# Optimization experiments

Measured on AMD Instinct MI355X. Metric: run time of the kernel, lower is better.

Reference implementation:

```python
import jax, jax.numpy as jnp
import numpy as np

DIM = 512
NUM_HEADS = 8
HEAD_DIM = DIM // NUM_HEADS
SCALE = HEAD_DIM ** -0.5


def setup_inputs() -> dict:
    key = jax.random.key(0)
    kx, kqw, kqb, kpw, kpb = jax.random.split(key, 5)
    B, N = 2, 4096
    x = jax.random.normal(kx, (B, N, DIM), dtype=jnp.float32)
    # nn.Linear weights stored as [out, in]; init ~ U(-1/sqrt(in), 1/sqrt(in))
    bound = 1.0 / np.sqrt(DIM)
    qkv_w = jax.random.uniform(kqw, (3 * DIM, DIM), minval=-bound, maxval=bound, dtype=jnp.float32)
    qkv_b = jax.random.uniform(kqb, (3 * DIM,), minval=-bound, maxval=bound, dtype=jnp.float32)
    proj_w = jax.random.uniform(kpw, (DIM, DIM), minval=-bound, maxval=bound, dtype=jnp.float32)
    proj_b = jax.random.uniform(kpb, (DIM,), minval=-bound, maxval=bound, dtype=jnp.float32)
    return {"x": x, "qkv_w": qkv_w, "qkv_b": qkv_b, "proj_w": proj_w, "proj_b": proj_b}


def reference(x, qkv_w, qkv_b, proj_w, proj_b):
    B, N, C = x.shape
    # qkv: [B, N, 3C] -> [3, B, H, N, Dh]
    qkv = x @ qkv_w.T + qkv_b
    qkv = qkv.reshape(B, N, 3, NUM_HEADS, HEAD_DIM).transpose(2, 0, 3, 1, 4)
    q, k, v = qkv[0], qkv[1], qkv[2]
    # scores: [B, H, N, N] (materialized, matching the original math)
    attn = jnp.einsum("bhqd,bhkd->bhqk", q, k) * SCALE
    attn = jax.nn.softmax(attn, axis=-1)
    out = jnp.einsum("bhqk,bhkd->bhqd", attn, v)  # [B, H, N, Dh]
    out = out.transpose(0, 2, 1, 3).reshape(B, N, C)
    return out @ proj_w.T + proj_b
```

## Files before the change

kernel.cpp:

```cpp
#include <hip/hip_runtime.h>
#include <hip/hip_bf16.h>
#include <stdint.h>
#include <stddef.h>

typedef __attribute__((ext_vector_type(8))) short short8;
typedef __attribute__((ext_vector_type(4))) float f32x4;
typedef __attribute__((ext_vector_type(16))) float f32x16;

#define MFMA16(a, b, c) __builtin_amdgcn_mfma_f32_16x16x32_bf16((a), (b), (c), 0, 0, 0)
#define MFMA32(a, b, c) __builtin_amdgcn_mfma_f32_32x32x16_bf16((a), (b), (c), 0, 0, 0)

#define QSCALE 0.1803368801111204f

#if __has_builtin(__builtin_amdgcn_exp2f)
#define EXP2(x) __builtin_amdgcn_exp2f(x)
#else
#define EXP2(x) __builtin_exp2f(x)
#endif

__device__ __forceinline__ float b2f(short x) {
    unsigned u = ((unsigned)(unsigned short)x) << 16;
    float f; __builtin_memcpy(&f, &u, 4); return f;
}
__device__ __forceinline__ short f2b(float f) {
    unsigned u; __builtin_memcpy(&u, &f, 4);
    u = (u + 0x7FFFu + ((u >> 16) & 1u)) >> 16;
    return (short)u;
}
__device__ __forceinline__ unsigned pack2(float a, float b) {
    unsigned ua, ub; __builtin_memcpy(&ua, &a, 4); __builtin_memcpy(&ub, &b, 4);
    return __builtin_amdgcn_perm(ub + 0x8000u, ua + 0x8000u, 0x07060302u);
}
__device__ __forceinline__ unsigned cvtpk(float a, float b) {
    unsigned r;
    asm("v_cvt_pk_bf16_f32 %0, %1, %2" : "=v"(r) : "v"(a), "v"(b));
    return r;
}
__device__ __forceinline__ short8 load8f(const float* p) {
    const float4 f0 = *(const float4*)p;
    const float4 f1 = *(const float4*)(p + 4);
    short8 r;
    r[0]=f2b(f0.x); r[1]=f2b(f0.y); r[2]=f2b(f0.z); r[3]=f2b(f0.w);
    r[4]=f2b(f1.x); r[5]=f2b(f1.y); r[6]=f2b(f1.z); r[7]=f2b(f1.w);
    return r;
}

__global__ __launch_bounds__(256) void cvt3(
    const float* __restrict__ s0, short* __restrict__ d0, int n0,
    const float* __restrict__ s1, short* __restrict__ d1, int n1,
    const float* __restrict__ s2, short* __restrict__ d2, int n2)
{
    int i = blockIdx.x * 256 + threadIdx.x;
    if (i < n0) { *(short8*)(d0 + (size_t)i * 8) = load8f(s0 + (size_t)i * 8); return; }
    i -= n0;
    if (i < n1) { *(short8*)(d1 + (size_t)i * 8) = load8f(s1 + (size_t)i * 8); return; }
    i -= n1;
    if (i < n2) { *(short8*)(d2 + (size_t)i * 8) = load8f(s2 + (size_t)i * 8); }
}

__global__ __launch_bounds__(256) void qkv_gemm(
    const short* __restrict__ X, const short* __restrict__ W,
    const float* __restrict__ bias,
    short* __restrict__ Qb, short* __restrict__ Kb, short* __restrict__ Vb)
{
    __shared__ short sT[128][132];

    const int tid  = threadIdx.x;
    const int wv   = tid >> 6;
    const int lane = tid & 63;
    const int l15  = lane & 15;
    const int quad = lane >> 4;
    const int m0   = blockIdx.x * 128 + (wv >> 1) * 64;
    const int sec  = blockIdx.y >> 2;
    const int bis  = blockIdx.y & 3;
    const int nbase = sec * 512 + bis * 128;
    const int j0   = (wv & 1) * 64;

    const f32x4 zero = {0.f, 0.f, 0.f, 0.f};
    f32x4 acc[4][4];
#pragma unroll
    for (int i = 0; i < 4; i++)
#pragma unroll
        for (int j = 0; j < 4; j++) acc[i][j] = zero;

    for (int k0 = 0; k0 < 512; k0 += 32) {
        short8 a[4], b[4];
#pragma unroll
        for (int i = 0; i < 4; i++)
            a[i] = *(const short8*)(X + (size_t)(m0 + i * 16 + l15) * 512 + k0 + quad * 8);
#pragma unroll
        for (int j = 0; j < 4; j++)
            b[j] = *(const short8*)(W + (size_t)(nbase + j0 + j * 16 + l15) * 512 + k0 + quad * 8);
#pragma unroll
        for (int i = 0; i < 4; i++)
#pragma unroll
            for (int j = 0; j < 4; j++)
                acc[i][j] = MFMA16(a[i], b[j], acc[i][j]);
    }

    if (sec < 2) {
        const float scale = (sec == 0) ? QSCALE : 1.0f;
        short* dst = (sec == 0) ? Qb : Kb;
#pragma unroll
        for (int j = 0; j < 4; j++) {
            const int jcl = j0 + j * 16 + l15;
            const float bs = bias[sec * 512 + bis * 128 + jcl];
#pragma unroll
            for (int i = 0; i < 4; i++) {
                const int s0 = (wv >> 1) * 64 + i * 16 + quad * 4;
#pragma unroll
                for (int r = 0; r < 4; r++)
                    sT[s0 + r][jcl] = f2b((acc[i][j][r] + bs) * scale);
            }
        }
        __syncthreads();

        const int seqlocal = tid & 127;
        const int hl_loc   = tid >> 7;
        const int hl  = bis * 2 + hl_loc;
        const int m   = blockIdx.x * 128 + seqlocal;
        const int bb  = m >> 12, seqg = m & 4095;
        short* drow = dst + ((size_t)(bb * 8 + hl) * 4096 + seqg) * 64;
#pragma unroll
        for (int u = 0; u < 8; u++)
            *(short8*)(drow + u * 8) = *(const short8*)&sT[seqlocal][hl_loc * 64 + u * 8];
    } else {
#pragma unroll
        for (int j = 0; j < 4; j++) {
            const int jcl = j0 + j * 16 + l15;
            const float bs = bias[nbase + jcl];
#pragma unroll
            for (int i = 0; i < 4; i++) {
                uint2 w;
                w.x = pack2(acc[i][j][0] + bs, acc[i][j][1] + bs);
                w.y = pack2(acc[i][j][2] + bs, acc[i][j][3] + bs);
                *(uint2*)&sT[jcl][(wv >> 1) * 64 + i * 16 + quad * 4] = w;
            }
        }
        __syncthreads();

        const int jcl = tid >> 1, half = tid & 1;
        const int hl = (bis * 128 + jcl) >> 6;
        const int d  = jcl & 63;
        const int bb = (blockIdx.x * 128) >> 12;
        const int seq0 = ((blockIdx.x * 128) & 4095) + half * 64;
        short* dst = Vb + ((size_t)(bb * 8 + hl) * 64 + d) * 4096 + seq0;
#pragma unroll
        for (int u = 0; u < 8; u++)
            *(short8*)(dst + u * 8) = *(const short8*)&sT[jcl][half * 64 + u * 8];
    }
}

__global__ __launch_bounds__(512, 4) void flash_attn(
    const short* __restrict__ Q, const short* __restrict__ K,
    const short* __restrict__ V, short* __restrict__ PO0,
    short* __restrict__ PO1, float* __restrict__ lbuf, int niter)
{
    __shared__ short sK[2][128][72];
    __shared__ short sV[2][64][136];

    const int tid  = threadIdx.x;
    const int wv   = tid >> 6;
    const int lane = tid & 63;
    const int l31  = lane & 31;
    const int half = lane >> 5;
    const int bh = blockIdx.y;
    const int b = bh >> 3, h = bh & 7;
    const int qw = blockIdx.x * 256 + wv * 32;
    const int ks = blockIdx.z;
    const int key0 = ks * niter * 128;

    const short* Qb = Q + (size_t)bh * 4096 * 64;
    const short* Kb = K + (size_t)bh * 4096 * 64;
    const short* Vb = V + (size_t)bh * 64 * 4096;

    short8 aq[4];
#pragma unroll
    for (int s = 0; s < 4; s++)
        aq[s] = *(const short8*)(Qb + (size_t)(qw + l31) * 64 + s * 16 + half * 8);

    f32x16 o0 = {}, o1 = {};
    float la0 = 0.f, la1 = 0.f, la2 = 0.f, la3 = 0.f;

    const int r0  = tid >> 3;
    const int scb = (tid & 7) * 8;
    const int vb  = (scb & ~12) | ((scb & 8) >> 1);

    short8 pk0, pk1, pv0, pv1;
    pk0 = *(const short8*)(Kb + (size_t)(key0 + r0) * 64 + scb);
    pk1 = *(const short8*)(Kb + (size_t)(key0 + 64 + r0) * 64 + scb);
    pv0 = *(const short8*)(Vb + (size_t)r0 * 4096 + key0 + scb);
    pv1 = *(const short8*)(Vb + (size_t)r0 * 4096 + key0 + 64 + scb);
    *(short8*)&sK[0][r0][scb]      = pk0;
    *(short8*)&sK[0][64 + r0][scb] = pk1;
    *(uint2*)&sV[0][r0][vb]          = ((const uint2*)&pv0)[0];
    *(uint2*)&sV[0][r0][vb + 8]      = ((const uint2*)&pv0)[1];
    *(uint2*)&sV[0][r0][64 + vb]     = ((const uint2*)&pv1)[0];
    *(uint2*)&sV[0][r0][64 + vb + 8] = ((const uint2*)&pv1)[1];
    {
        const int kn = key0 + 128;
        pk0 = *(const short8*)(Kb + (size_t)(kn + r0) * 64 + scb);
        pk1 = *(const short8*)(Kb + (size_t)(kn + 64 + r0) * 64 + scb);
        pv0 = *(const short8*)(Vb + (size_t)r0 * 4096 + kn + scb);
        pv1 = *(const short8*)(Vb + (size_t)r0 * 4096 + kn + 64 + scb);
    }

    for (int kt = 0; kt < niter; ++kt) {
        __syncthreads();

        if (kt + 1 < niter) {
            short (*sKn)[72]  = sK[(kt + 1) & 1];
            short (*sVn)[136] = sV[(kt + 1) & 1];
            *(short8*)&sKn[r0][scb]      = pk0;
            *(short8*)&sKn[64 + r0][scb] = pk1;
            *(uint2*)&sVn[r0][vb]          = ((const uint2*)&pv0)[0];
            *(uint2*)&sVn[r0][vb + 8]      = ((const uint2*)&pv0)[1];
            *(uint2*)&sVn[r0][64 + vb]     = ((const uint2*)&pv1)[0];
            *(uint2*)&sVn[r0][64 + vb + 8] = ((const uint2*)&pv1)[1];
        }
        if (kt + 2 < niter) {
            const int kn = key0 + (kt + 2) * 128;
            pk0 = *(const short8*)(Kb + (size_t)(kn + r0) * 64 + scb);
            pk1 = *(const short8*)(Kb + (size_t)(kn + 64 + r0) * 64 + scb);
            pv0 = *(const short8*)(Vb + (size_t)r0 * 4096 + kn + scb);
            pv1 = *(const short8*)(Vb + (size_t)r0 * 4096 + kn + 64 + scb);
        }

        const short (*sKc)[72]  = sK[kt & 1];
        const short (*sVc)[136] = sV[kt & 1];

#pragma unroll
        for (int i = 0; i < 4; i++) {
            const int c = (i + wv) & 3;
            f32x16 ST = {};
            __builtin_amdgcn_s_setprio(1);
#pragma unroll
            for (int s = 0; s < 4; s++) {
                const short8 bk = *(const short8*)&sKc[c * 32 + l31][s * 16 + half * 8];
                ST = MFMA32(bk, aq[s], ST);
            }
            __builtin_amdgcn_s_setprio(0);
            float e[16];
#pragma unroll
            for (int r = 0; r < 16; r++) e[r] = EXP2(ST[r]);
            la0 += (e[0] + e[1]) + (e[2] + e[3]);
            la1 += (e[4] + e[5]) + (e[6] + e[7]);
            la2 += (e[8] + e[9]) + (e[10] + e[11]);
            la3 += (e[12] + e[13]) + (e[14] + e[15]);
            uint4 w0 = { cvtpk(e[0], e[1]),   cvtpk(e[2], e[3]),
                         cvtpk(e[4], e[5]),   cvtpk(e[6], e[7]) };
            uint4 w1 = { cvtpk(e[8], e[9]),   cvtpk(e[10], e[11]),
                         cvtpk(e[12], e[13]), cvtpk(e[14], e[15]) };
            const short8 bp0 = *(const short8*)&w0;
            const short8 bp1 = *(const short8*)&w1;

            __builtin_amdgcn_s_setprio(1);
            const short8 bv00 = *(const short8*)&sVc[l31][(2 * c) * 16 + half * 8];
            const short8 bv01 = *(const short8*)&sVc[32 + l31][(2 * c) * 16 + half * 8];
            o0 = MFMA32(bv00, bp0, o0);
            o1 = MFMA32(bv01, bp0, o1);
            const short8 bv10 = *(const short8*)&sVc[l31][(2 * c + 1) * 16 + half * 8];
            const short8 bv11 = *(const short8*)&sVc[32 + l31][(2 * c + 1) * 16 + half * 8];
            o0 = MFMA32(bv10, bp1, o0);
            o1 = MFMA32(bv11, bp1, o1);
            __builtin_amdgcn_s_setprio(0);
        }
    }

    float lsum = (la0 + la1) + (la2 + la3);
    lsum += __shfl_xor(lsum, 32);
    const float inv = 1.f / fmaxf(lsum, 1e-30f);

    short* PO = (ks == 0) ? PO0 : PO1;
#pragma unroll
    for (int q = 0; q < 4; q++) {
        uint2 w0, w1;
        w0.x = pack2(o0[4 * q + 0] * inv, o0[4 * q + 1] * inv);
        w0.y = pack2(o0[4 * q + 2] * inv, o0[4 * q + 3] * inv);
        w1.x = pack2(o1[4 * q + 0] * inv, o1[4 * q + 1] * inv);
        w1.y = pack2(o1[4 * q + 2] * inv, o1[4 * q + 3] * inv);
        const size_t rowoff = ((size_t)b * 4096 + qw + l31) * 512;
        const int col = h * 64 + q * 8 + half * 4;
        *(uint2*)(PO + rowoff + col) = w0;
        *(uint2*)(PO + rowoff + col + 32) = w1;
    }
    if (half == 0)
        lbuf[((size_t)ks * 16 + bh) * 4096 + qw + l31] = lsum;
}

__global__ __launch_bounds__(256) void combine(
    const short* __restrict__ PO0, const short* __restrict__ PO1,
    short* __restrict__ attn, const float* __restrict__ L)
{
    const int i = blockIdx.x * 256 + threadIdx.x;
    const size_t flat = (size_t)i * 8;
    const int col = (int)(flat & 511);
    const int q   = (int)((flat >> 9) & 4095);
    const int b   = (int)(flat >> 21);
    const int bh  = b * 8 + (col >> 6);
    const float l0 = L[(size_t)bh * 4096 + q];
    const float l1 = L[(size_t)65536 + (size_t)bh * 4096 + q];
    const float inv = 1.f / (l0 + l1);
    const float w0 = l0 * inv, w1 = l1 * inv;
    const short8 a = *(const short8*)(PO0 + flat);
    const short8 c = *(const short8*)(PO1 + flat);
    short8 r;
#pragma unroll
    for (int k = 0; k < 8; k += 2) {
        const unsigned p = pack2(w0 * b2f(a[k]) + w1 * b2f(c[k]),
                                 w0 * b2f(a[k + 1]) + w1 * b2f(c[k + 1]));
        r[k]     = (short)(p & 0xFFFF);
        r[k + 1] = (short)(p >> 16);
    }
    *(short8*)(attn + flat) = r;
}

__global__ __launch_bounds__(256) void proj_gemm(
    const short* __restrict__ A, const short* __restrict__ W,
    const float* __restrict__ bias, float* __restrict__ dst)
{
    const int tid  = threadIdx.x;
    const int wv   = tid >> 6;
    const int lane = tid & 63;
    const int l15  = lane & 15;
    const int quad = lane >> 4;
    const int m0 = blockIdx.x * 128 + (wv >> 1) * 64;
    const int n0 = blockIdx.y * 128 + (wv & 1) * 64;

    const f32x4 zero = {0.f, 0.f, 0.f, 0.f};
    f32x4 acc[4][4];
#pragma unroll
    for (int i = 0; i < 4; i++)
#pragma unroll
        for (int j = 0; j < 4; j++) acc[i][j] = zero;

    for (int k0 = 0; k0 < 512; k0 += 32) {
        short8 a[4], b[4];
#pragma unroll
        for (int i = 0; i < 4; i++)
            a[i] = *(const short8*)(A + (size_t)(m0 + i * 16 + l15) * 512 + k0 + quad * 8);
#pragma unroll
        for (int j = 0; j < 4; j++)
            b[j] = *(const short8*)(W + (size_t)(n0 + j * 16 + l15) * 512 + k0 + quad * 8);
#pragma unroll
        for (int i = 0; i < 4; i++)
#pragma unroll
            for (int j = 0; j < 4; j++)
                acc[i][j] = MFMA16(a[i], b[j], acc[i][j]);
    }

#pragma unroll
    for (int j = 0; j < 4; j++) {
        const int n = n0 + j * 16 + l15;
        const float bs = bias[n];
#pragma unroll
        for (int i = 0; i < 4; i++) {
#pragma unroll
            for (int r = 0; r < 4; r++) {
                const int m = m0 + i * 16 + quad * 4 + r;
                dst[(size_t)m * 512 + n] = acc[i][j][r] + bs;
            }
        }
    }
}

extern "C" void kernel_launch(void* const* d_in, const int* in_sizes, int n_in,
                              void* d_out, int out_size, void* d_ws, size_t ws_size,
                              hipStream_t stream)
{
    const float* x      = (const float*)d_in[0];
    const float* qkv_w  = (const float*)d_in[1];
    const float* qkv_b  = (const float*)d_in[2];
    const float* proj_w = (const float*)d_in[3];
    const float* proj_b = (const float*)d_in[4];

    const size_t MB = 1024 * 1024;
    short* xb   = (short*)d_out;
    short* wb   = (short*)d_out + 4 * MB;
    short* PO0  = (short*)d_out;
    short* PO1  = (short*)d_out + 4 * MB;
    float* out  = (float*)d_out;

    short* Qf = (short*)d_ws;
    short* Kf = Qf + (size_t)16 * 4096 * 64;
    short* Vf = Kf + (size_t)16 * 4096 * 64;
    short* attn = Qf;
    float* lbuf = (float*)((char*)d_ws + 24 * MB);
    short* pwb  = (short*)((char*)d_ws + 24 * MB + 512 * 1024);

    cvt3<<<2560, 256, 0, stream>>>(x, xb, 524288, qkv_w, wb, 98304, proj_w, pwb, 32768);
    qkv_gemm<<<dim3(64, 12), 256, 0, stream>>>(xb, wb, qkv_b, Qf, Kf, Vf);
    flash_attn<<<dim3(16, 16, 2), 512, 0, stream>>>(Qf, Kf, Vf, PO0, PO1, lbuf, 16);
    combine<<<2048, 256, 0, stream>>>(PO0, PO1, attn, lbuf);
    proj_gemm<<<dim3(64, 4), 256, 0, stream>>>(attn, pwb, proj_b, out);
}
```

Baseline: 230.6 us.

## Prefetch GEMM operands, compute softmax row sums via MFMA, retile projection GEMM

Both GEMM kernels now load the next k-slice's operands into registers before issuing the current MFMAs, so global load latency overlaps with compute. The flash attention kernel drops its scalar row-sum accumulation and shuffle, and instead sums the probabilities with an extra MFMA against a vector of bf16 ones. The projection GEMM uses smaller 64x128 tiles, twice as many blocks, and swapped MFMA operands so each lane writes float4 outputs with vectorized bias loads. The costs are higher register pressure from double-buffered operands, extra MFMA work in the attention inner loop, and a row sum taken from bf16-rounded probabilities rather than fp32 values.

```diff
diff --git a/kernel.cpp b/kernel.cpp
--- a/kernel.cpp
+++ b/kernel.cpp
@@ -83,19 +83,32 @@
 #pragma unroll
         for (int j = 0; j < 4; j++) acc[i][j] = zero;
 
+    const short* Arow = X + (size_t)(m0 + l15) * 512 + quad * 8;
+    const short* Brow = W + (size_t)(nbase + j0 + l15) * 512 + quad * 8;
+
+    short8 a[4], b[4];
+#pragma unroll
+    for (int i = 0; i < 4; i++) a[i] = *(const short8*)(Arow + (size_t)i * 16 * 512);
+#pragma unroll
+    for (int j = 0; j < 4; j++) b[j] = *(const short8*)(Brow + (size_t)j * 16 * 512);
+
+#pragma unroll 2
     for (int k0 = 0; k0 < 512; k0 += 32) {
-        short8 a[4], b[4];
-#pragma unroll
-        for (int i = 0; i < 4; i++)
-            a[i] = *(const short8*)(X + (size_t)(m0 + i * 16 + l15) * 512 + k0 + quad * 8);
-#pragma unroll
-        for (int j = 0; j < 4; j++)
-            b[j] = *(const short8*)(W + (size_t)(nbase + j0 + j * 16 + l15) * 512 + k0 + quad * 8);
+        const int kn = (k0 + 32 < 512) ? k0 + 32 : 0;
+        short8 an[4], bn[4];
+#pragma unroll
+        for (int i = 0; i < 4; i++) an[i] = *(const short8*)(Arow + (size_t)i * 16 * 512 + kn);
+#pragma unroll
+        for (int j = 0; j < 4; j++) bn[j] = *(const short8*)(Brow + (size_t)j * 16 * 512 + kn);
 #pragma unroll
         for (int i = 0; i < 4; i++)
 #pragma unroll
             for (int j = 0; j < 4; j++)
                 acc[i][j] = MFMA16(a[i], b[j], acc[i][j]);
+#pragma unroll
+        for (int i = 0; i < 4; i++) a[i] = an[i];
+#pragma unroll
+        for (int j = 0; j < 4; j++) b[j] = bn[j];
     }
 
     if (sec < 2) {
@@ -179,8 +192,12 @@
     for (int s = 0; s < 4; s++)
         aq[s] = *(const short8*)(Qb + (size_t)(qw + l31) * 64 + s * 16 + half * 8);
 
+    short8 ones;
+#pragma unroll
+    for (int j = 0; j < 8; j++) ones[j] = (short)0x3F80;
+
     f32x16 o0 = {}, o1 = {};
-    float la0 = 0.f, la1 = 0.f, la2 = 0.f, la3 = 0.f;
+    f32x16 o2 = {};
 
     const int r0  = tid >> 3;
     const int scb = (tid & 7) * 8;
@@ -243,10 +260,6 @@
             float e[16];
 #pragma unroll
             for (int r = 0; r < 16; r++) e[r] = EXP2(ST[r]);
-            la0 += (e[0] + e[1]) + (e[2] + e[3]);
-            la1 += (e[4] + e[5]) + (e[6] + e[7]);
-            la2 += (e[8] + e[9]) + (e[10] + e[11]);
-            la3 += (e[12] + e[13]) + (e[14] + e[15]);
             uint4 w0 = { cvtpk(e[0], e[1]),   cvtpk(e[2], e[3]),
                          cvtpk(e[4], e[5]),   cvtpk(e[6], e[7]) };
             uint4 w1 = { cvtpk(e[8], e[9]),   cvtpk(e[10], e[11]),
@@ -259,16 +272,17 @@
             const short8 bv01 = *(const short8*)&sVc[32 + l31][(2 * c) * 16 + half * 8];
             o0 = MFMA32(bv00, bp0, o0);
             o1 = MFMA32(bv01, bp0, o1);
+            o2 = MFMA32(ones, bp0, o2);
             const short8 bv10 = *(const short8*)&sVc[l31][(2 * c + 1) * 16 + half * 8];
             const short8 bv11 = *(const short8*)&sVc[32 + l31][(2 * c + 1) * 16 + half * 8];
             o0 = MFMA32(bv10, bp1, o0);
             o1 = MFMA32(bv11, bp1, o1);
+            o2 = MFMA32(ones, bp1, o2);
             __builtin_amdgcn_s_setprio(0);
         }
     }
 
-    float lsum = (la0 + la1) + (la2 + la3);
-    lsum += __shfl_xor(lsum, 32);
+    const float lsum = o2[0];
     const float inv = 1.f / fmaxf(lsum, 1e-30f);
 
     short* PO = (ks == 0) ? PO0 : PO1;
@@ -324,42 +338,57 @@
     const int lane = tid & 63;
     const int l15  = lane & 15;
     const int quad = lane >> 4;
-    const int m0 = blockIdx.x * 128 + (wv >> 1) * 64;
-    const int n0 = blockIdx.y * 128 + (wv & 1) * 64;
+    const int m0 = blockIdx.x * 64;
+    const int n0 = blockIdx.y * 128 + wv * 32;
 
     const f32x4 zero = {0.f, 0.f, 0.f, 0.f};
-    f32x4 acc[4][4];
+    f32x4 acc[4][2];
 #pragma unroll
     for (int i = 0; i < 4; i++)
 #pragma unroll
-        for (int j = 0; j < 4; j++) acc[i][j] = zero;
-
+        for (int j = 0; j < 2; j++) acc[i][j] = zero;
+
+    const short* Arow = A + (size_t)(m0 + l15) * 512 + quad * 8;
+    const short* Brow = W + (size_t)(n0 + l15) * 512 + quad * 8;
+
+    short8 a[4], b[2];
+#pragma unroll
+    for (int i = 0; i < 4; i++) a[i] = *(const short8*)(Arow + (size_t)i * 16 * 512);
+#pragma unroll
+    for (int j = 0; j < 2; j++) b[j] = *(const short8*)(Brow + (size_t)j * 16 * 512);
+
+#pragma unroll 2
     for (int k0 = 0; k0 < 512; k0 += 32) {
-        short8 a[4], b[4];
+        const int kn = (k0 + 32 < 512) ? k0 + 32 : 0;
+        short8 an[4], bn[2];
+#pragma unroll
+        for (int i = 0; i < 4; i++) an[i] = *(const short8*)(Arow + (size_t)i * 16 * 512 + kn);
+#pragma unroll
+        for (int j = 0; j < 2; j++) bn[j] = *(const short8*)(Brow + (size_t)j * 16 * 512 + kn);
 #pragma unroll
         for (int i = 0; i < 4; i++)
-            a[i] = *(const short8*)(A + (size_t)(m0 + i * 16 + l15) * 512 + k0 + quad * 8);
-#pragma unroll
-        for (int j = 0; j < 4; j++)
-            b[j] = *(const short8*)(W + (size_t)(n0 + j * 16 + l15) * 512 + k0 + quad * 8);
-#pragma unroll
-        for (int i = 0; i < 4; i++)
-#pragma unroll
-            for (int j = 0; j < 4; j++)
-                acc[i][j] = MFMA16(a[i], b[j], acc[i][j]);
-    }
-
-#pragma unroll
-    for (int j = 0; j < 4; j++) {
-        const int n = n0 + j * 16 + l15;
-        const float bs = bias[n];
-#pragma unroll
-        for (int i = 0; i < 4; i++) {
-#pragma unroll
-            for (int r = 0; r < 4; r++) {
-                const int m = m0 + i * 16 + quad * 4 + r;
-                dst[(size_t)m * 512 + n] = acc[i][j][r] + bs;
-            }
+#pragma unroll
+            for (int j = 0; j < 2; j++)
+                acc[i][j] = MFMA16(b[j], a[i], acc[i][j]);
+#pragma unroll
+        for (int i = 0; i < 4; i++) a[i] = an[i];
+#pragma unroll
+        for (int j = 0; j < 2; j++) b[j] = bn[j];
+    }
+
+#pragma unroll
+    for (int i = 0; i < 4; i++) {
+        const int m = m0 + i * 16 + l15;
+#pragma unroll
+        for (int j = 0; j < 2; j++) {
+            const int n = n0 + j * 16 + quad * 4;
+            const float4 bs = *(const float4*)(bias + n);
+            float4 o;
+            o.x = acc[i][j][0] + bs.x;
+            o.y = acc[i][j][1] + bs.y;
+            o.z = acc[i][j][2] + bs.z;
+            o.w = acc[i][j][3] + bs.w;
+            *(float4*)(dst + (size_t)m * 512 + n) = o;
         }
     }
 }
@@ -392,5 +421,5 @@
     qkv_gemm<<<dim3(64, 12), 256, 0, stream>>>(xb, wb, qkv_b, Qf, Kf, Vf);
     flash_attn<<<dim3(16, 16, 2), 512, 0, stream>>>(Qf, Kf, Vf, PO0, PO1, lbuf, 16);
     combine<<<2048, 256, 0, stream>>>(PO0, PO1, attn, lbuf);
-    proj_gemm<<<dim3(64, 4), 256, 0, stream>>>(attn, pwb, proj_b, out);
-}
+    proj_gemm<<<dim3(128, 4), 256, 0, stream>>>(attn, pwb, proj_b, out);
+}
```

New measurement: 235.4 us. +2.1%, slower.
